# Performance work log

Hardware: AMD Instinct MI355X
Metric: run time of the kernel (lower is better)

The kernel has to match this reference:

```python
import jax, jax.numpy as jnp
import numpy as np

ALPHA = 0.2  # LeakyReLU negative slope


def setup_inputs() -> dict:
    key = jax.random.key(0)
    k1, k2, k3, k4 = jax.random.split(key, 4)
    B, N, F_in, F_out = 16, 2048, 64, 64
    h = jax.random.normal(k1, (B, N, F_in), dtype=jnp.float32)
    bias_mat = jnp.zeros((B, N, N), dtype=jnp.float32)
    # xavier_uniform with gain=1.414
    def xavier(k, shape, gain=1.414):
        fan_in, fan_out = shape[0], shape[1]
        bound = gain * np.sqrt(6.0 / (fan_in + fan_out))
        return jax.random.uniform(k, shape, jnp.float32, -bound, bound)
    W = xavier(k2, (F_in, F_out))
    a1 = xavier(k3, (F_out, 1))
    a2 = xavier(k4, (F_out, 1))
    return {"h": h, "bias_mat": bias_mat, "W": W, "a1": a1, "a2": a2}


def reference(h, bias_mat, W, a1, a2):
    # h: [B, N, F_in]; W: [F_in, F_out]
    Wh = jnp.einsum("bnf,fo->bno", h, W)            # [B, N, F_out]
    Wh1 = jnp.einsum("bno,oi->bni", Wh, a1)          # [B, N, 1]
    Wh2 = jnp.einsum("bno,oi->bni", Wh, a2)          # [B, N, 1]
    e = Wh1 + jnp.swapaxes(Wh2, 1, 2)                # [B, N, N] additive scores
    e = jax.nn.leaky_relu(e, negative_slope=ALPHA) + bias_mat
    attention = jax.nn.softmax(e, axis=2)            # row-wise over neighbors
    h_prime = jnp.einsum("bnm,bmo->bno", attention, Wh)
    return h_prime
```

## Files before the change

kernel.cpp:

```cpp
#include <hip/hip_runtime.h>
#include <hip/hip_bf16.h>
#include <cstdint>
#include <cstddef>

#define ALPHA 0.2f
#define LOG2E 1.4426950408889634f

using f32x4 = __attribute__((ext_vector_type(4))) float;
using s16x8 = __attribute__((ext_vector_type(8))) short;

typedef __attribute__((address_space(3))) unsigned lds_u32;
typedef __attribute__((address_space(1))) const unsigned glb_u32;

__device__ __forceinline__ unsigned f2bf(float f) {
  unsigned u = __float_as_uint(f);
  u = (u + 0x7fffu + ((u >> 16) & 1u)) >> 16;
  return u;
}

#define FENCE asm volatile("" ::: "memory")

__global__ __launch_bounds__(256) void k1_proj(
    const float* __restrict__ h, const float* __restrict__ W,
    const float* __restrict__ a1, const float* __restrict__ a2,
    unsigned short* __restrict__ whT, float* __restrict__ s1,
    float* __restrict__ s2) {
  __shared__ __align__(16) char h_lds[64 * 256];
  __shared__ __align__(16) float W_lds[64 * 64];
  __shared__ __align__(16) unsigned short t_lds[64 * 64];
  __shared__ float red[4][64][2];

  const int t = threadIdx.x;
  const int l = t & 63;
  const int w = t >> 6;
  const int rq = l & 15;
  const int cq = w * 4 + (l >> 4);
  const int c0 = cq * 4;
  const int row0 = blockIdx.x * 64;

  const float4* hg = (const float4*)(h + (size_t)row0 * 64);
  #pragma unroll
  for (int r = 0; r < 4; ++r) {
    const int f = t + r * 256;
    const int n = f >> 4, ch = f & 15;
    *(float4*)(h_lds + n * 256 + ((ch * 16) ^ (((n >> 2) & 7) << 4))) = hg[f];
    ((float4*)W_lds)[f] = ((const float4*)W)[f];
  }
  const f32x4 a1v = *(const f32x4*)(a1 + c0);
  const f32x4 a2v = *(const f32x4*)(a2 + c0);
  __syncthreads();

  f32x4 acc[4];
  #pragma unroll
  for (int i = 0; i < 4; ++i) acc[i] = (f32x4){0.f, 0.f, 0.f, 0.f};

  #pragma unroll 1
  for (int kc = 0; kc < 16; ++kc) {
    f32x4 wv[4];
    #pragma unroll
    for (int kk = 0; kk < 4; ++kk)
      wv[kk] = *(const f32x4*)(W_lds + (kc * 4 + kk) * 64 + c0);
    #pragma unroll
    for (int i = 0; i < 4; ++i) {
      const int n = rq * 4 + i;
      const f32x4 hv = *(const f32x4*)(
          h_lds + n * 256 + ((kc * 16) ^ (((n >> 2) & 7) << 4)));
      #pragma unroll
      for (int j = 0; j < 4; ++j) {
        acc[i][j] = fmaf(hv[0], wv[0][j], acc[i][j]);
        acc[i][j] = fmaf(hv[1], wv[1][j], acc[i][j]);
        acc[i][j] = fmaf(hv[2], wv[2][j], acc[i][j]);
        acc[i][j] = fmaf(hv[3], wv[3][j], acc[i][j]);
      }
    }
  }

  float p1[4], p2[4];
  #pragma unroll
  for (int i = 0; i < 4; ++i) {
    p1[i] = acc[i][0] * a1v[0] + acc[i][1] * a1v[1] + acc[i][2] * a1v[2] +
            acc[i][3] * a1v[3];
    p2[i] = acc[i][0] * a2v[0] + acc[i][1] * a2v[1] + acc[i][2] * a2v[2] +
            acc[i][3] * a2v[3];
    p1[i] += __shfl_xor(p1[i], 16, 64);
    p1[i] += __shfl_xor(p1[i], 32, 64);
    p2[i] += __shfl_xor(p2[i], 16, 64);
    p2[i] += __shfl_xor(p2[i], 32, 64);
  }
  if (l < 16) {
    #pragma unroll
    for (int i = 0; i < 4; ++i) {
      red[w][rq * 4 + i][0] = p1[i];
      red[w][rq * 4 + i][1] = p2[i];
    }
  }

  #pragma unroll
  for (int j = 0; j < 4; ++j) {
    const int c = c0 + j;
    uint2 u;
    u.x = f2bf(acc[0][j]) | (f2bf(acc[1][j]) << 16);
    u.y = f2bf(acc[2][j]) | (f2bf(acc[3][j]) << 16);
    *(uint2*)((char*)t_lds + c * 128 + ((rq * 8) ^ ((c & 7) << 4))) = u;
  }
  __syncthreads();

  const int b = row0 >> 11;
  const int n0 = row0 & 2047;
  #pragma unroll
  for (int q = 0; q < 2; ++q) {
    const int chunk = q * 256 + t;
    const int cc = chunk >> 3;
    const int w8 = (chunk & 7) * 16;
    const uint4 v =
        *(const uint4*)((const char*)t_lds + cc * 128 + (w8 ^ ((cc & 7) << 4)));
    *(uint4*)((char*)whT + ((size_t)(b * 64 + cc) * 2048 + n0) * 2 + w8) = v;
  }
  if (t < 128) {
    const int n = t >> 1, v = t & 1;
    const float s =
        red[0][n][v] + red[1][n][v] + red[2][n][v] + red[3][n][v];
    if (v == 0)
      s1[row0 + n] = s;
    else
      s2[row0 + n] = s;
  }
}

__global__ __launch_bounds__(256, 2) void k2_attn(
    const float* __restrict__ bias, const unsigned short* __restrict__ whT,
    const float* __restrict__ s1g, const float* __restrict__ s2g,
    float* __restrict__ out) {
  __shared__ __align__(16) unsigned short wbuf[4][4096];
  __shared__ __align__(16) float s2_lds[2048];

  const int t = threadIdx.x;
  const int lane = t & 63;
  const int w = t >> 6;
  const int arow = lane & 15;
  const int kgrp = lane >> 4;
  const int b = blockIdx.x >> 5;
  const int i0 = (blockIdx.x & 31) * 64;
  const int gi = i0 + w * 16 + arow;

  const float s1v = s1g[b * 2048 + gi];

  #pragma unroll
  for (int q = 0; q < 2; ++q)
    ((float4*)s2_lds)[t + q * 256] =
        ((const float4*)(s2g + b * 2048))[t + q * 256];
  __syncthreads();

  const char* whT_b = (const char*)whT + (size_t)b * 64 * 2048 * 2;
  const float* bias_p = bias + ((size_t)b * 2048 + gi) * 2048 + kgrp * 8;

  const int src_swz = ((lane & 7) * 16) ^ ((lane >> 3) << 4);
  const char* gsrc0 = whT_b + (size_t)(lane >> 3) * 4096 + src_swz;

  auto whT_gll = [&](int jt) {
    char* dst = (char*)wbuf + (jt & 3) * 8192;
    #pragma unroll
    for (int q = 0; q < 2; ++q) {
      const int chunk = w * 2 + q;
      __builtin_amdgcn_global_load_lds(
          (glb_u32*)(gsrc0 + (size_t)chunk * 8 * 4096 + jt * 128),
          (lds_u32*)(dst + chunk * 1024), 16, 0, 0);
    }
  };
  auto bias_load = [&](f32x4 (&dst)[4], int jt) {
    const float* p = bias_p + jt * 64;
    dst[0] = *(const f32x4*)(p);
    dst[1] = *(const f32x4*)(p + 4);
    dst[2] = *(const f32x4*)(p + 32);
    dst[3] = *(const f32x4*)(p + 36);
  };

  f32x4 acc[4];
  #pragma unroll
  for (int ct = 0; ct < 4; ++ct) acc[ct] = (f32x4){0.f, 0.f, 0.f, 0.f};
  float l = 0.0f;

  f32x4 biasA[4], biasB[4];
  bias_load(biasA, 0);
  FENCE;
  whT_gll(0);
  whT_gll(1);
  FENCE;
  bias_load(biasB, 1);
  FENCE;

  auto body = [&](int jt, f32x4 (&bcur)[4]) {
    if (jt + 2 < 32) whT_gll(jt + 2);
    FENCE;

    float ps = 0.0f;
    s16x8 afrag[2];
    #pragma unroll
    for (int f = 0; f < 2; ++f) {
      const f32x4 sa = *(const f32x4*)(s2_lds + jt * 64 + f * 32 + kgrp * 8);
      const f32x4 sb =
          *(const f32x4*)(s2_lds + jt * 64 + f * 32 + kgrp * 8 + 4);
      const f32x4 ba = bcur[f * 2 + 0];
      const f32x4 bb = bcur[f * 2 + 1];
      #pragma unroll
      for (int e = 0; e < 4; ++e) {
        float x = s1v + sa[e];
        x = fmaxf(x, ALPHA * x);
        const float p = exp2f((x + ba[e]) * LOG2E);
        ps += p;
        float y = s1v + sb[e];
        y = fmaxf(y, ALPHA * y);
        const float q = exp2f((y + bb[e]) * LOG2E);
        ps += q;
        afrag[f][e] = (short)f2bf(p);
        afrag[f][e + 4] = (short)f2bf(q);
      }
    }
    l += ps;

    if (jt + 2 < 32) bias_load(bcur, jt + 2);
    FENCE;

    asm volatile("s_waitcnt vmcnt(12)" ::: "memory");
    asm volatile("s_barrier" ::: "memory");

    const char* mybuf = (const char*)wbuf + (jt & 3) * 8192;
    #pragma unroll
    for (int ct = 0; ct < 4; ++ct) {
      const int cc = ct * 16 + arow;
      #pragma unroll
      for (int f = 0; f < 2; ++f) {
        const s16x8 bfrag = *(const s16x8*)(
            mybuf + cc * 128 + ((f * 64 + kgrp * 16) ^ ((cc & 7) << 4)));
        asm("s_nop 1\n\t"
            "v_mfma_f32_16x16x32_bf16 %0, %1, %2, %0"
            : "+v"(acc[ct])
            : "v"(afrag[f]), "v"(bfrag));
      }
    }
  };

  #pragma unroll 1
  for (int jt = 0; jt < 32; jt += 2) {
    body(jt + 0, biasA);
    body(jt + 1, biasB);
  }

  asm volatile("s_nop 7\n\ts_nop 7" ::: "memory");

  l += __shfl_xor(l, 16, 64);
  l += __shfl_xor(l, 32, 64);
  const float linv = 1.0f / l;
  #pragma unroll
  for (int r = 0; r < 4; ++r) {
    const float li = __shfl(linv, kgrp * 4 + r, 64);
    float* op = out + ((size_t)b * 2048 + i0 + w * 16 + kgrp * 4 + r) * 64;
    #pragma unroll
    for (int ct = 0; ct < 4; ++ct) op[ct * 16 + arow] = acc[ct][r] * li;
  }
}

extern "C" void kernel_launch(void* const* d_in, const int* in_sizes, int n_in,
                              void* d_out, int out_size, void* d_ws,
                              size_t ws_size, hipStream_t stream) {
  const float* h = (const float*)d_in[0];
  const float* bias = (const float*)d_in[1];
  const float* W = (const float*)d_in[2];
  const float* a1 = (const float*)d_in[3];
  const float* a2 = (const float*)d_in[4];
  float* out = (float*)d_out;

  char* ws = (char*)d_ws;
  unsigned short* whT = (unsigned short*)ws;
  float* s1 = (float*)(ws + 4 * 1024 * 1024);
  float* s2 = (float*)(ws + 4 * 1024 * 1024 + 128 * 1024);

  k1_proj<<<dim3(512), dim3(256), 0, stream>>>(h, W, a1, a2, whT, s1, s2);
  k2_attn<<<dim3(512), dim3(256), 0, stream>>>(bias, whT, s1, s2, out);
}
```

Before: 68.05 us.

## Split attention key range across two wave groups per block, combine via LDS

The attention block grows from 256 to 512 threads. Each group of four waves handles half of the 2048 neighbour columns, using its own set of LDS staging buffers. When both halves finish, the second half writes its partial accumulators and row sums to LDS, and the first half adds them in, normalises and stores the output. The goal is twice as many resident waves per CU, so more bias and Wh loads are in flight to hide memory latency. The cost is more LDS per block, an extra reduction step, and a possible race from reusing the second half's staging buffer as the combine scratch.

```diff
diff --git a/kernel.cpp b/kernel.cpp
--- a/kernel.cpp
+++ b/kernel.cpp
@@ -127,28 +127,28 @@
   }
 }
 
-__global__ __launch_bounds__(256, 2) void k2_attn(
+__global__ __launch_bounds__(512, 4) void k2_attn(
     const float* __restrict__ bias, const unsigned short* __restrict__ whT,
     const float* __restrict__ s1g, const float* __restrict__ s2g,
     float* __restrict__ out) {
-  __shared__ __align__(16) unsigned short wbuf[4][4096];
+  __shared__ __align__(16) unsigned short wbuf[2][4][4096];
   __shared__ __align__(16) float s2_lds[2048];
 
   const int t = threadIdx.x;
   const int lane = t & 63;
   const int w = t >> 6;
+  const int half = w >> 2;
+  const int wl = w & 3;
   const int arow = lane & 15;
   const int kgrp = lane >> 4;
   const int b = blockIdx.x >> 5;
   const int i0 = (blockIdx.x & 31) * 64;
-  const int gi = i0 + w * 16 + arow;
+  const int gi = i0 + wl * 16 + arow;
+  const int jbase = half * 16;
 
   const float s1v = s1g[b * 2048 + gi];
 
-  #pragma unroll
-  for (int q = 0; q < 2; ++q)
-    ((float4*)s2_lds)[t + q * 256] =
-        ((const float4*)(s2g + b * 2048))[t + q * 256];
+  ((float4*)s2_lds)[t] = ((const float4*)(s2g + b * 2048))[t];
   __syncthreads();
 
   const char* whT_b = (const char*)whT + (size_t)b * 64 * 2048 * 2;
@@ -157,18 +157,18 @@
   const int src_swz = ((lane & 7) * 16) ^ ((lane >> 3) << 4);
   const char* gsrc0 = whT_b + (size_t)(lane >> 3) * 4096 + src_swz;
 
-  auto whT_gll = [&](int jt) {
-    char* dst = (char*)wbuf + (jt & 3) * 8192;
+  auto whT_gll = [&](int it) {
+    char* dst = (char*)wbuf[half] + (it & 3) * 8192;
     #pragma unroll
     for (int q = 0; q < 2; ++q) {
-      const int chunk = w * 2 + q;
+      const int chunk = wl * 2 + q;
       __builtin_amdgcn_global_load_lds(
-          (glb_u32*)(gsrc0 + (size_t)chunk * 8 * 4096 + jt * 128),
+          (glb_u32*)(gsrc0 + (size_t)chunk * 8 * 4096 + (jbase + it) * 128),
           (lds_u32*)(dst + chunk * 1024), 16, 0, 0);
     }
   };
-  auto bias_load = [&](f32x4 (&dst)[4], int jt) {
-    const float* p = bias_p + jt * 64;
+  auto bias_load = [&](f32x4 (&dst)[4], int it) {
+    const float* p = bias_p + (jbase + it) * 64;
     dst[0] = *(const f32x4*)(p);
     dst[1] = *(const f32x4*)(p + 4);
     dst[2] = *(const f32x4*)(p + 32);
@@ -189,17 +189,18 @@
   bias_load(biasB, 1);
   FENCE;
 
-  auto body = [&](int jt, f32x4 (&bcur)[4]) {
-    if (jt + 2 < 32) whT_gll(jt + 2);
+  auto body = [&](int it, f32x4 (&bcur)[4]) {
+    if (it + 2 < 16) whT_gll(it + 2);
     FENCE;
 
     float ps = 0.0f;
     s16x8 afrag[2];
     #pragma unroll
     for (int f = 0; f < 2; ++f) {
-      const f32x4 sa = *(const f32x4*)(s2_lds + jt * 64 + f * 32 + kgrp * 8);
+      const f32x4 sa =
+          *(const f32x4*)(s2_lds + (jbase + it) * 64 + f * 32 + kgrp * 8);
       const f32x4 sb =
-          *(const f32x4*)(s2_lds + jt * 64 + f * 32 + kgrp * 8 + 4);
+          *(const f32x4*)(s2_lds + (jbase + it) * 64 + f * 32 + kgrp * 8 + 4);
       const f32x4 ba = bcur[f * 2 + 0];
       const f32x4 bb = bcur[f * 2 + 1];
       #pragma unroll
@@ -218,13 +219,13 @@
     }
     l += ps;
 
-    if (jt + 2 < 32) bias_load(bcur, jt + 2);
+    if (it + 2 < 16) bias_load(bcur, it + 2);
     FENCE;
 
     asm volatile("s_waitcnt vmcnt(12)" ::: "memory");
     asm volatile("s_barrier" ::: "memory");
 
-    const char* mybuf = (const char*)wbuf + (jt & 3) * 8192;
+    const char* mybuf = (const char*)wbuf[half] + (it & 3) * 8192;
     #pragma unroll
     for (int ct = 0; ct < 4; ++ct) {
       const int cc = ct * 16 + arow;
@@ -241,22 +242,38 @@
   };
 
   #pragma unroll 1
-  for (int jt = 0; jt < 32; jt += 2) {
-    body(jt + 0, biasA);
-    body(jt + 1, biasB);
+  for (int it = 0; it < 16; it += 2) {
+    body(it + 0, biasA);
+    body(it + 1, biasB);
   }
 
   asm volatile("s_nop 7\n\ts_nop 7" ::: "memory");
 
-  l += __shfl_xor(l, 16, 64);
-  l += __shfl_xor(l, 32, 64);
-  const float linv = 1.0f / l;
-  #pragma unroll
-  for (int r = 0; r < 4; ++r) {
-    const float li = __shfl(linv, kgrp * 4 + r, 64);
-    float* op = out + ((size_t)b * 2048 + i0 + w * 16 + kgrp * 4 + r) * 64;
-    #pragma unroll
-    for (int ct = 0; ct < 4; ++ct) op[ct * 16 + arow] = acc[ct][r] * li;
+  float* combuf = (float*)wbuf[1];
+  const int idx = wl * 64 + lane;
+  if (half == 1) {
+    #pragma unroll
+    for (int ct = 0; ct < 4; ++ct)
+      *(f32x4*)(combuf + idx * 17 + ct * 4) = acc[ct];
+    combuf[idx * 17 + 16] = l;
+  }
+  __syncthreads();
+  if (half == 0) {
+    #pragma unroll
+    for (int ct = 0; ct < 4; ++ct)
+      acc[ct] += *(const f32x4*)(combuf + idx * 17 + ct * 4);
+    l += combuf[idx * 17 + 16];
+
+    l += __shfl_xor(l, 16, 64);
+    l += __shfl_xor(l, 32, 64);
+    const float linv = 1.0f / l;
+    #pragma unroll
+    for (int r = 0; r < 4; ++r) {
+      const float li = __shfl(linv, kgrp * 4 + r, 64);
+      float* op = out + ((size_t)b * 2048 + i0 + wl * 16 + kgrp * 4 + r) * 64;
+      #pragma unroll
+      for (int ct = 0; ct < 4; ++ct) op[ct * 16 + arow] = acc[ct][r] * li;
+    }
   }
 }
 
@@ -276,5 +293,5 @@
   float* s2 = (float*)(ws + 4 * 1024 * 1024 + 128 * 1024);
 
   k1_proj<<<dim3(512), dim3(256), 0, stream>>>(h, W, a1, a2, whT, s1, s2);
-  k2_attn<<<dim3(512), dim3(256), 0, stream>>>(bias, whT, s1, s2, out);
-}
+  k2_attn<<<dim3(512), dim3(512), 0, stream>>>(bias, whT, s1, s2, out);
+}
```

Measured after the change: 68.66 us. No clear change (+0.9%).
